# Optimization experiments

Hardware: AMD Instinct MI355X
Metric: run time of the kernel (lower is better)

Reference implementation:

```python
import math
import jax, jax.numpy as jnp
import numpy as np

DIM = 128
BASE = 10000.0
MAX_POS = 4096
SCALING = 4.0
BETA_FAST = 32
BETA_SLOW = 1
EXTRAP = 1.0
ATTN_FACTOR = 1.0
SEQ_LEN = 16384
HIDDEN = 2048
BATCH = 2


def _find_correction_dim(num_rot, dim, base, max_pos):
    return dim * math.log(max_pos / (num_rot * 2 * math.pi)) / (2 * math.log(base))


def _yarn_buffers():
    # replicates ResonanceYaRNScalingRotaryEmbedding.__init__ buffer math
    pos_freqs = BASE ** (np.arange(0, DIM, 2, dtype=np.float32) / DIM)
    inv_freq_extrap = 1.0 / pos_freqs
    inv_freq_interp = 1.0 / (SCALING * pos_freqs)
    low = math.floor(_find_correction_dim(BETA_FAST, DIM, BASE, MAX_POS))
    high = math.ceil(_find_correction_dim(BETA_SLOW, DIM, BASE, MAX_POS))
    low, high = max(low, 0), min(high, DIM - 1)
    if low == high:
        high += 0.001
    ramp = np.clip((np.arange(DIM // 2, dtype=np.float32) - low) / (high - low), 0.0, 1.0)
    inv_freq_mask = (1.0 - ramp) * EXTRAP
    inv_freq = inv_freq_interp * (1.0 - inv_freq_mask) + inv_freq_extrap * inv_freq_mask
    r_wavelengths = np.round(2.0 * math.pi / inv_freq)
    r_inv_freq = (2.0 * math.pi / r_wavelengths).astype(np.float32)
    return jnp.asarray(r_inv_freq), jnp.asarray(r_wavelengths.astype(np.float32))


MSCALE = float((0.1 * math.log(SCALING) + 1.0) * ATTN_FACTOR)


def setup_inputs() -> dict:
    key = jax.random.key(0)
    x = jax.random.normal(key, (BATCH, SEQ_LEN, HIDDEN), dtype=jnp.float32)
    position_ids = jnp.arange(SEQ_LEN, dtype=jnp.int64 if jax.config.jax_enable_x64 else jnp.int32)[None, :]
    r_inv_freq, r_wavelengths = _yarn_buffers()
    return {"x": x, "position_ids": position_ids, "r_inv_freq": r_inv_freq, "r_wavelengths": r_wavelengths}


def reference(x, position_ids, r_inv_freq, r_wavelengths):
    # The per-frequency python loop (tile first `wavelength` positions to seq_len)
    # is equivalent to indexing position_ids at (l % wavelength_i): when
    # seq_len >= w the repeat+slice realizes exactly pos[l % w]; when w > seq_len,
    # l % w == l, matching the else branch. One modulo gather replaces the loop.
    L = position_ids.shape[1]
    wav_i = r_wavelengths.astype(jnp.int32)                    # (D/2,)
    idx = jnp.arange(L, dtype=jnp.int32)[:, None] % wav_i[None, :]  # (L, D/2)
    pos_mod = jnp.take(position_ids, idx, axis=1).astype(jnp.float32)  # (B, L, D/2)
    freqs = pos_mod * r_inv_freq                               # (B, L, D/2)
    emb = jnp.concatenate([freqs, freqs], axis=-1)             # (B, L, D)
    cos = (jnp.cos(emb) * MSCALE).astype(x.dtype)
    sin = (jnp.sin(emb) * MSCALE).astype(x.dtype)
    return cos, sin
```

## Files before the change

### kernel.cpp

```cpp
#include <hip/hip_runtime.h>

#define MSCALE 1.1386294361119891f


__global__ void yarn_rope_kernel(const int* __restrict__ pos_ids,
                                 const float* __restrict__ inv_freq,
                                 const float* __restrict__ wavelengths,
                                 float* __restrict__ out,
                                 int L, long long sin_off) {
    int gid = blockIdx.x * blockDim.x + threadIdx.x;
    int d = gid & 63;
    int l = gid >> 6;
    if (l >= L) return;

    int   w   = (int)wavelengths[d];
    float ifr = inv_freq[d];

    int idx = l % w;
    float pos = (float)pos_ids[idx];
    float f = pos * ifr;

    float c = cosf(f) * MSCALE;
    float s = sinf(f) * MSCALE;

    long long base = (long long)l * 128 + d;
    out[base]           = c;
    out[base + 64]      = c;
    out[sin_off + base]       = s;
    out[sin_off + base + 64]  = s;
}

extern "C" void kernel_launch(void* const* d_in, const int* in_sizes, int n_in,
                              void* d_out, int out_size, void* d_ws, size_t ws_size,
                              hipStream_t stream) {
    const int*   pos_ids = (const int*)d_in[1];
    const float* inv_freq = (const float*)d_in[2];
    const float* wav      = (const float*)d_in[3];
    float* out = (float*)d_out;

    int L = in_sizes[1];
    long long sin_off = (long long)out_size / 2;

    int total = L * 64;
    int block = 256;
    int grid = (total + block - 1) / block;
    yarn_rope_kernel<<<grid, block, 0, stream>>>(pos_ids, inv_freq, wav, out, L, sin_off);
}
```

Before: 300.0 us.

## Vectorize RoPE stores, use fast sincos, and amortize modulo across rows

Each thread now handles four frequencies and two sequence rows. It loads the frequency and wavelength buffers as float4 and writes the cos/sin outputs as float4 stores. The exact cosf/sinf calls become __sincosf, and per-element integer modulo becomes an incrementing wrapped index. This cuts instruction count and store transactions, and avoids the slow-path argument reduction of the precise trig functions. It relies on arguments staying within about 2π, which holds because pos < wavelength. It also narrows offsets to 32-bit ints, which limits the output size that can be addressed.

```diff
diff --git a/kernel.cpp b/kernel.cpp
--- a/kernel.cpp
+++ b/kernel.cpp
@@ -1,48 +1,70 @@
 #include <hip/hip_runtime.h>
 
 #define MSCALE 1.1386294361119891f
+#define RPT 2
 
 
-__global__ void yarn_rope_kernel(const int* __restrict__ pos_ids,
-                                 const float* __restrict__ inv_freq,
-                                 const float* __restrict__ wavelengths,
-                                 float* __restrict__ out,
-                                 int L, long long sin_off) {
-    int gid = blockIdx.x * blockDim.x + threadIdx.x;
-    int d = gid & 63;
-    int l = gid >> 6;
-    if (l >= L) return;
+__global__ __launch_bounds__(256) void yarn_rope_kernel(
+        const int*   __restrict__ pos_ids,
+        const float* __restrict__ inv_freq,
+        const float* __restrict__ wavelengths,
+        float*       __restrict__ out,
+        int L, int sin_off) {
+    int t = threadIdx.x;
+    int g = t & 15;
+    int r = t >> 4;
+    int l0 = (blockIdx.x * 16 + r) * RPT;
+    if (l0 >= L) return;
+    int d = g * 4;
 
-    int   w   = (int)wavelengths[d];
-    float ifr = inv_freq[d];
+    float4 ifr = *(const float4*)(inv_freq + d);
+    float4 wv  = *(const float4*)(wavelengths + d);
+    int w0 = (int)wv.x, w1 = (int)wv.y, w2 = (int)wv.z, w3 = (int)wv.w;
 
-    int idx = l % w;
-    float pos = (float)pos_ids[idx];
-    float f = pos * ifr;
+    int i0 = l0 % w0, i1 = l0 % w1, i2 = l0 % w2, i3 = l0 % w3;
 
-    float c = cosf(f) * MSCALE;
-    float s = sinf(f) * MSCALE;
+    #pragma unroll
+    for (int k = 0; k < RPT; ++k) {
+        int l = l0 + k;
 
-    long long base = (long long)l * 128 + d;
-    out[base]           = c;
-    out[base + 64]      = c;
-    out[sin_off + base]       = s;
-    out[sin_off + base + 64]  = s;
+        float f0 = (float)pos_ids[i0] * ifr.x;
+        float f1 = (float)pos_ids[i1] * ifr.y;
+        float f2 = (float)pos_ids[i2] * ifr.z;
+        float f3 = (float)pos_ids[i3] * ifr.w;
+
+        float4 c, s;
+        __sincosf(f0, &s.x, &c.x);
+        __sincosf(f1, &s.y, &c.y);
+        __sincosf(f2, &s.z, &c.z);
+        __sincosf(f3, &s.w, &c.w);
+        c.x *= MSCALE; c.y *= MSCALE; c.z *= MSCALE; c.w *= MSCALE;
+        s.x *= MSCALE; s.y *= MSCALE; s.z *= MSCALE; s.w *= MSCALE;
+
+        int base = l * 128 + d;
+        *(float4*)(out + base)                = c;
+        *(float4*)(out + base + 64)           = c;
+        *(float4*)(out + sin_off + base)      = s;
+        *(float4*)(out + sin_off + base + 64) = s;
+
+        i0 = (i0 + 1 == w0) ? 0 : i0 + 1;
+        i1 = (i1 + 1 == w1) ? 0 : i1 + 1;
+        i2 = (i2 + 1 == w2) ? 0 : i2 + 1;
+        i3 = (i3 + 1 == w3) ? 0 : i3 + 1;
+    }
 }
 
 extern "C" void kernel_launch(void* const* d_in, const int* in_sizes, int n_in,
                               void* d_out, int out_size, void* d_ws, size_t ws_size,
                               hipStream_t stream) {
-    const int*   pos_ids = (const int*)d_in[1];
+    const int*   pos_ids  = (const int*)d_in[1];
     const float* inv_freq = (const float*)d_in[2];
     const float* wav      = (const float*)d_in[3];
     float* out = (float*)d_out;
 
     int L = in_sizes[1];
-    long long sin_off = (long long)out_size / 2;
+    int sin_off = out_size / 2;
 
-    int total = L * 64;
-    int block = 256;
-    int grid = (total + block - 1) / block;
-    yarn_rope_kernel<<<grid, block, 0, stream>>>(pos_ids, inv_freq, wav, out, L, sin_off);
+    int rows_per_block = 16 * RPT;
+    int grid = (L + rows_per_block - 1) / rows_per_block;
+    yarn_rope_kernel<<<grid, 256, 0, stream>>>(pos_ids, inv_freq, wav, out, L, sin_off);
 }
```

Measured after the change: 298.9 us. No clear change (-0.4%).
